# Kernel optimization log

Hardware: AMD Instinct MI355X
Metric: run time of the kernel (lower is better)

Reference implementation:

```python
import jax, jax.numpy as jnp
import numpy as np

B, NVIS, NPIX, W = 16, 65536, 1024, 64
NBLOCKS = NVIS // W
NITER = 10


def setup_inputs() -> dict:
    key = jax.random.key(0)
    ks = jax.random.split(key, 10)
    s = 1.0 / np.sqrt(W)  # torch Linear default init range
    return {
        "y_re": jax.random.normal(ks[0], (B, NVIS), jnp.float32),
        "y_im": jax.random.normal(ks[1], (B, NVIS), jnp.float32),
        "H_re": jax.random.normal(ks[2], (NVIS, NPIX), jnp.float32) / np.sqrt(NPIX),
        "H_im": jax.random.normal(ks[3], (NVIS, NPIX), jnp.float32) / np.sqrt(NPIX),
        "estep_w": jax.random.uniform(ks[4], (W, W), jnp.float32, -s, s),
        "estep_b": jax.random.uniform(ks[5], (W,), jnp.float32, -s, s),
        "update_w": jax.random.uniform(ks[6], (W, W), jnp.float32, -s, s),
        "update_b": jax.random.uniform(ks[7], (W,), jnp.float32, -s, s),
        "memory_w": jax.random.uniform(ks[8], (W, W), jnp.float32, -s, s),
        "memory_b": jax.random.uniform(ks[9], (W,), jnp.float32, -s, s),
        "threshold": jnp.float32(0.001),
        "niter": NITER,
    }


def _forward(y_re, y_im, H_re, H_im, estep_w, estep_b, update_w, update_b,
             memory_w, memory_b, threshold, niter):
    w = estep_w.shape[0]                       # net_width
    batch, nvis = y_re.shape
    nblocks = nvis // w
    y = (y_re + 1j * y_im).reshape(batch, nblocks, w)          # [B, K, W] complex
    H = (H_re + 1j * H_im).reshape(nblocks, w, -1)             # [K, W, P] complex
    npix = H.shape[-1]

    # x0 = sum over blocks of y_k @ H_k  -> [B, P]
    x = jnp.einsum('bkw,kwp->bp', y, H)
    tau = jnp.zeros((batch, nblocks, w), jnp.float32)

    y_k = jnp.swapaxes(y, 0, 1)                                # [K, B, W]

    def block_step(x, inputs):
        Hb, yb, tprev = inputs                                 # [W,P], [B,W], [B,W]
        zk = jnp.einsum('bp,wp->bw', x, Hb.conj())             # [B, W] complex
        r2 = jnp.abs(yb - zk) ** 2                             # [B, W] float
        ht = jax.nn.sigmoid(r2 @ estep_w.T + estep_b)
        wnew = jax.nn.relu(ht @ update_w.T + update_b
                           + tprev @ memory_w.T + memory_b)    # [B, W] float
        zk = zk * wnew.astype(zk.dtype)
        x = x + jnp.einsum('bw,wp->bp', yb - zk, Hb) / w       # residual back-projection
        return x, wnew

    for _ in range(niter):
        tau_k = jnp.swapaxes(tau, 0, 1)                        # [K, B, W]
        x, tau_new = jax.lax.scan(block_step, x, (H, y_k, tau_k))
        tau = jnp.swapaxes(tau_new, 0, 1)
        # global soft-threshold: sgn(x) * relu(|x| - threshold * max|x|)
        absx = jnp.abs(x)
        mag = jax.nn.relu(absx - threshold * jnp.max(absx))
        safe = jnp.where(absx > 0, absx, 1.0)
        sgn = jnp.where(absx > 0, x / safe, 0.0 + 0.0j)
        x = sgn * mag

    return jnp.abs(x)                                          # [B, P] float


def reference(y_re, y_im, H_re, H_im, estep_w, estep_b, update_w, update_b,
              memory_w, memory_b, threshold, niter):
    return _forward(y_re, y_im, H_re, H_im, estep_w, estep_b, update_w,
                    update_b, memory_w, memory_b, threshold, niter)
```

## Files before the change

kernel.cpp:

```cpp
#include <hip/hip_runtime.h>
#include <math.h>

#define NB     16
#define NW     64
#define NK     1024
#define NPX    1024
#define NVIS_  65536
#define NMEM   15
#define TPB    256
#define NWG    256
#define NQP    19

#define WS_ROOTA   0
#define WS_ROOTB   16
#define WS_GMAX    288
#define WS_SRING_W 2048
#define WS_RRING_W 493568
#define WS_X0P_W   526336
#define WS_TAU_W   1574912
#define WS_G_W     2623488
#define INIT_W     526336

#define AG_LDF(p)    __hip_atomic_load((p), __ATOMIC_RELAXED, __HIP_MEMORY_SCOPE_AGENT)
#define AG_STF(p,v)  __hip_atomic_store((p), (v), __ATOMIC_RELAXED, __HIP_MEMORY_SCOPE_AGENT)
#define AG_STU(p,v)  __hip_atomic_store((p), (v), __ATOMIC_RELAXED, __HIP_MEMORY_SCOPE_AGENT)
#define AG_ST64(p,v) __hip_atomic_store((p), (v), __ATOMIC_RELAXED, __HIP_MEMORY_SCOPE_AGENT)

#define BARL() do { asm volatile("s_waitcnt lgkmcnt(0)" ::: "memory"); \
                    __builtin_amdgcn_s_barrier(); } while (0)

typedef struct { float re[NW][NQP][4]; float im[NW][NQP][4]; } HTile;
typedef struct {
  HTile tile[3];
  float xs[160];
  float rs[128];
  float partl[128];
  float red[8][NQP][8];
  float axs[128];
} MemSM;
typedef struct {
  float wE[NW*65], wU[NW*65], wM[NW*65];
  float bE[NW], bU[NW], bM[NW];
  float ztA[128], ztB[128];
  float rloc[2][128];
  float rpost[128];
  float r2s[NW], tpl[NW], hts[NW];
} SeqSM;
typedef struct { float ysr[2048], ysi[2048]; } X0SM;
typedef union { MemSM m; SeqSM q; X0SM x; } SMem;

__global__ void robbi_init(unsigned* ws) {
  for (int i = blockIdx.x * blockDim.x + threadIdx.x; i < INIT_W; i += gridDim.x * blockDim.x)
    __hip_atomic_store(ws + i, 0u, __ATOMIC_RELAXED, __HIP_MEMORY_SCOPE_AGENT);
}

__device__ __forceinline__ void gbar(unsigned* root, unsigned* leaf, int leafmod, unsigned ntarget) {
  __syncthreads();
  if (threadIdx.x == 0) {
    unsigned old = __hip_atomic_fetch_add(leaf, 1u, __ATOMIC_ACQ_REL, __HIP_MEMORY_SCOPE_AGENT);
    if ((old % (unsigned)leafmod) == (unsigned)(leafmod - 1))
      __hip_atomic_fetch_add(root, 1u, __ATOMIC_ACQ_REL, __HIP_MEMORY_SCOPE_AGENT);
    while (__hip_atomic_load(root, __ATOMIC_ACQUIRE, __HIP_MEMORY_SCOPE_AGENT) < ntarget)
      __builtin_amdgcn_s_sleep(4);
  }
  __syncthreads();
}

__global__ __launch_bounds__(256) void robbi_gram(const float* __restrict__ H_re,
                                                  const float* __restrict__ H_im,
                                                  float* ws) {
  const int j = blockIdx.x >> 1;
  const int d = (blockIdx.x & 1) + 1;
  const int k = j + d;
  if (k >= NK) return;
  unsigned* Gu = (unsigned*)ws + WS_G_W;
  const int t = threadIdx.x;
  __shared__ float hj[64 * 130];
  __shared__ float hk[64 * 130];
  const int c = t & 63, wg = t >> 6;
  float accr[16], acci[16];
#pragma unroll
  for (int ii = 0; ii < 16; ++ii) { accr[ii] = 0.f; acci[ii] = 0.f; }
  for (int pc = 0; pc < 16; ++pc) {
    for (int q = t; q < 1024; q += 256) {
      int row = q >> 4, px4 = (q & 15) * 4;
      size_t offj = (size_t)(j * NW + row) * NPX + pc * 64 + px4;
      size_t offk = (size_t)(k * NW + row) * NPX + pc * 64 + px4;
      float4 r4 = *(const float4*)(H_re + offj);
      float4 i4 = *(const float4*)(H_im + offj);
      int b0 = row * 130 + px4 * 2;
      hj[b0+0]=r4.x; hj[b0+1]=i4.x; hj[b0+2]=r4.y; hj[b0+3]=i4.y;
      hj[b0+4]=r4.z; hj[b0+5]=i4.z; hj[b0+6]=r4.w; hj[b0+7]=i4.w;
      r4 = *(const float4*)(H_re + offk);
      i4 = *(const float4*)(H_im + offk);
      hk[b0+0]=r4.x; hk[b0+1]=i4.x; hk[b0+2]=r4.y; hk[b0+3]=i4.y;
      hk[b0+4]=r4.z; hk[b0+5]=i4.z; hk[b0+6]=r4.w; hk[b0+7]=i4.w;
    }
    __syncthreads();
#pragma unroll
    for (int ii = 0; ii < 16; ++ii) {
      const int w = wg * 16 + ii;
      float ar_ = 0.f, ai_ = 0.f;
      for (int px = 0; px < 64; ++px) {
        float jr = hj[w*130 + px*2], ji = hj[w*130 + px*2 + 1];
        float kr = hk[c*130 + px*2], ki = hk[c*130 + px*2 + 1];
        ar_ += jr*kr + ji*ki;
        ai_ += ji*kr - jr*ki;
      }
      accr[ii] += ar_; acci[ii] += ai_;
    }
    __syncthreads();
  }
#pragma unroll
  for (int ii = 0; ii < 16; ++ii) {
    unsigned br = __float_as_uint(accr[ii]);
    br = (br + 0x7FFFu + ((br >> 16) & 1u)) & 0xFFFF0000u;
    unsigned bi = __float_as_uint(acci[ii]);
    bi = ((bi + 0x7FFFu + ((bi >> 16) & 1u)) >> 16) & 0xFFFFu;
    Gu[((size_t)(j * 2 + (d - 1)) * 64 + c) * 64 + wg * 16 + ii] = br | bi;
  }
}

#define GMAC(UU, IDX)                                                           \
  { unsigned uu_ = (UU);                                                        \
    float gr_ = __uint_as_float(uu_ & 0xffff0000u);                             \
    float gi_ = __uint_as_float(uu_ << 16);                                     \
    float rr_ = rl[2*(IDX)], ri_ = rl[2*(IDX)+1];                               \
    ar += rr_*gr_ - ri_*gi_; ai += rr_*gi_ + ri_*gr_; }

__global__ __launch_bounds__(TPB, 1) void robbi_pipe(
    const float* __restrict__ y_re, const float* __restrict__ y_im,
    const float* __restrict__ H_re, const float* __restrict__ H_im,
    const float* __restrict__ Ew, const float* __restrict__ Eb,
    const float* __restrict__ Uw, const float* __restrict__ Ub,
    const float* __restrict__ Mw, const float* __restrict__ Mb,
    const float* __restrict__ thr_p, const int* __restrict__ niter_p,
    float* __restrict__ out, float* ws) {
  const int bid = blockIdx.x;
  const int t = threadIdx.x;
  unsigned* wsu = (unsigned*)ws;
  const unsigned* Gu = wsu + WS_G_W;
  float* tau = ws + WS_TAU_W;
  __shared__ SMem sm;

  const float thr = *thr_p;
  const int niter = *niter_p;
  const int wsub = t >> 5;
  const int g5 = t & 31;
  const int p4 = 4 * g5;

  {
    const int kwc = bid >> 3, ps = bid & 7;
    float ar[2][4], ai[2][4];
#pragma unroll
    for (int h = 0; h < 2; ++h)
#pragma unroll
      for (int j = 0; j < 4; ++j) { ar[h][j] = 0.f; ai[h][j] = 0.f; }
    for (int slab = 0; slab < 16; ++slab) {
      const int kw0 = kwc * 2048 + slab * 128;
      for (int e = t; e < 2048; e += TPB) {
        int bb = e >> 7, j = e & 127;
        sm.x.ysr[e] = y_re[bb * NVIS_ + kw0 + j];
        sm.x.ysi[e] = y_im[bb * NVIS_ + kw0 + j];
      }
      __syncthreads();
      for (int j = 0; j < 128; ++j) {
        const size_t off2 = (size_t)(kw0 + j) * NPX + ps * 128 + p4;
        float4 h4r = *(const float4*)(H_re + off2);
        float4 h4i = *(const float4*)(H_im + off2);
#pragma unroll
        for (int h = 0; h < 2; ++h) {
          int bb = wsub + 8 * h;
          float yr = sm.x.ysr[bb * 128 + j], yi = sm.x.ysi[bb * 128 + j];
          ar[h][0] += yr*h4r.x - yi*h4i.x; ai[h][0] += yr*h4i.x + yi*h4r.x;
          ar[h][1] += yr*h4r.y - yi*h4i.y; ai[h][1] += yr*h4i.y + yi*h4r.y;
          ar[h][2] += yr*h4r.z - yi*h4i.z; ai[h][2] += yr*h4i.z + yi*h4r.z;
          ar[h][3] += yr*h4r.w - yi*h4i.w; ai[h][3] += yr*h4i.w + yi*h4r.w;
        }
      }
      __syncthreads();
    }
#pragma unroll
    for (int h = 0; h < 2; ++h) {
      int bb = wsub + 8 * h;
#pragma unroll
      for (int j = 0; j < 4; ++j) {
        float* pp = ws + WS_X0P_W + ((size_t)((kwc * NB + bb) * NPX + ps * 128 + p4 + j)) * 2;
        AG_STF(pp, ar[h][j]); AG_STF(pp + 1, ai[h][j]);
      }
    }
  }
  gbar(wsu + WS_ROOTA, wsu + 32 * (1 + (bid & 7)), 32, 8u);

  if (bid >= NB * NMEM) {
    const int b = bid - NB * NMEM;
    SeqSM* Q = &sm.q;
    for (int i = t; i < NW * NW; i += TPB) {
      int r = i >> 6, c = i & 63;
      Q->wE[r*65+c] = Ew[i]; Q->wU[r*65+c] = Uw[i]; Q->wM[r*65+c] = Mw[i];
    }
    if (t < NW) { Q->bE[t] = Eb[t]; Q->bU[t] = Ub[t]; Q->bM[t] = Mb[t]; }
    __syncthreads();
    if (niter <= 0) return;

    const int lane = t & 63;
    float ypr = 0.f, ypi = 0.f, tpr = 0.f;
    if (t < 64) { ypr = y_re[b * NVIS_ + t]; ypi = y_im[b * NVIS_ + t]; }
    uint4 g1[16], g2[16];
#pragma unroll
    for (int q2 = 0; q2 < 16; ++q2) { g1[q2] = make_uint4(0,0,0,0); g2[q2] = make_uint4(0,0,0,0); }

    const long NTOT = (long)niter * NK;
    for (long L = 0; L < NTOT; ++L) {
      const int k = (int)(L & (NK - 1));
      const int it2 = (int)(L >> 10);
      float zr = 0.f, zi = 0.f;
      if (t < 64) {
        const unsigned want = (unsigned)L + 1u;
        const int slot8 = (int)(L & 7);
        for (;;) {
          uint4 u[NMEM];
#pragma unroll
          for (int m2 = 0; m2 < NMEM; ++m2) {
            const uint4* p = (const uint4*)(wsu + WS_SRING_W +
              ((size_t)((b * 8 + slot8) * NMEM + m2) * 64 + t) * 4);
            asm volatile("global_load_dwordx4 %0, %1, off sc0 sc1" : "=v"(u[m2]) : "v"(p));
          }
          asm volatile("s_waitcnt vmcnt(0)" ::: "memory");
          __builtin_amdgcn_sched_barrier(0);
          bool ok = true; float ar = 0.f, ai = 0.f;
#pragma unroll
          for (int m2 = 0; m2 < NMEM; ++m2) {
            ok = ok && (u[m2].z == want);
            ar += __uint_as_float(u[m2].x); ai += __uint_as_float(u[m2].y);
          }
          if (__all((int)ok)) { zr = ar; zi = ai; break; }
          __builtin_amdgcn_s_sleep(1);
        }
      } else if (t < 128) {
        if (k >= 1) {
          const float* rl = Q->rloc[(int)((L - 1) & 1)];
          float ar = 0.f, ai = 0.f;
#pragma unroll
          for (int q2 = 0; q2 < 16; ++q2) {
            uint4 u = g1[q2];
            GMAC(u.x, 4*q2+0) GMAC(u.y, 4*q2+1) GMAC(u.z, 4*q2+2) GMAC(u.w, 4*q2+3)
          }
          Q->ztA[2*lane] = ar * (1.f / NW); Q->ztA[2*lane+1] = ai * (1.f / NW);
        }
      } else if (t < 192) {
        if (k >= 2) {
          const float* rl = Q->rloc[(int)((L - 2) & 1)];
          float ar = 0.f, ai = 0.f;
#pragma unroll
          for (int q2 = 0; q2 < 16; ++q2) {
            uint4 u = g2[q2];
            GMAC(u.x, 4*q2+0) GMAC(u.y, 4*q2+1) GMAC(u.z, 4*q2+2) GMAC(u.w, 4*q2+3)
          }
          Q->ztB[2*lane] = ar * (1.f / NW); Q->ztB[2*lane+1] = ai * (1.f / NW);
        }
      } else {
        if (k >= 1) {
          const unsigned Lr = (unsigned)(L - 1);
          union { float2 f2; unsigned long long u; } cv;
          cv.f2 = make_float2(Q->rpost[2*lane], Q->rpost[2*lane+1]);
          unsigned woff = WS_RRING_W + (((b * 8 + (int)(Lr & 7u)) * 64 + lane)) * 4;
          AG_ST64((unsigned long long*)(wsu + woff), cv.u);
          asm volatile("s_waitcnt vmcnt(0)" ::: "memory");
          AG_STU(wsu + woff + 2, Lr + 1u);
        }
      }
      BARL();
      if (t < 64) {
        float z_r = zr, z_i = zi;
        if (k >= 1) { z_r += Q->ztA[2*t]; z_i += Q->ztA[2*t+1]; }
        if (k >= 2) { z_r += Q->ztB[2*t]; z_i += Q->ztB[2*t+1]; }
        float dr = ypr - z_r, di = ypi - z_i;
        Q->r2s[t] = dr*dr + di*di;
        Q->tpl[t] = (it2 == 0) ? 0.f : tpr;
        asm volatile("s_waitcnt lgkmcnt(0)" ::: "memory");
        float e = Q->bE[t];
#pragma unroll 16
        for (int j2 = 0; j2 < 64; ++j2) e += Q->wE[t*65+j2] * Q->r2s[j2];
        Q->hts[t] = 1.f / (1.f + __expf(-e));
        asm volatile("s_waitcnt lgkmcnt(0)" ::: "memory");
        float a = Q->bU[t] + Q->bM[t];
#pragma unroll 16
        for (int j2 = 0; j2 < 64; ++j2)
          a += Q->wU[t*65+j2] * Q->hts[j2] + Q->wM[t*65+j2] * Q->tpl[j2];
        float wn = fmaxf(a, 0.f);
        tau[((size_t)b * NK + k) * NW + t] = wn;
        float rr = ypr - z_r * wn, ri = ypi - z_i * wn;
        Q->rloc[(int)(L & 1)][2*t] = rr; Q->rloc[(int)(L & 1)][2*t+1] = ri;
        Q->rpost[2*t] = rr; Q->rpost[2*t+1] = ri;
        if (L + 1 < NTOT) {
          const int k2 = (int)((L + 1) & (NK - 1));
          ypr = y_re[b * NVIS_ + k2 * NW + t];
          ypi = y_im[b * NVIS_ + k2 * NW + t];
          tpr = tau[((size_t)b * NK + k2) * NW + t];
        }
      } else if (t < 128) {
        if (k + 1 < NK) {
          const unsigned* gp = Gu + ((size_t)(k * 2 + 0) * 64 + lane) * 64;
#pragma unroll
          for (int q2 = 0; q2 < 16; ++q2) g1[q2] = ((const uint4*)gp)[q2];
        }
      } else if (t < 192) {
        if (k + 1 < NK && k >= 1) {
          const unsigned* gp = Gu + ((size_t)((k - 1) * 2 + 1) * 64 + lane) * 64;
#pragma unroll
          for (int q2 = 0; q2 < 16; ++q2) g2[q2] = ((const uint4*)gp)[q2];
        }
      }
      BARL();
      if (k == NK - 1 && t >= 192) {
        union { float2 f2; unsigned long long u; } cv;
        cv.f2 = make_float2(Q->rpost[2*lane], Q->rpost[2*lane+1]);
        unsigned woff = WS_RRING_W + (((b * 8 + (int)(L & 7u)) * 64 + lane)) * 4;
        AG_ST64((unsigned long long*)(wsu + woff), cv.u);
        asm volatile("s_waitcnt vmcnt(0)" ::: "memory");
        AG_STU(wsu + woff + 2, (unsigned)L + 1u);
      }
    }
    return;
  }

  const int b = bid / NMEM;
  const int m = bid % NMEM;
  const int off = m * 68;
  const int cnt = (m == NMEM - 1) ? 72 : 68;
  const int nq = cnt >> 2;
  MemSM* M = &sm.m;

  if (t < cnt * 2) {
    int p = t >> 1, c = t & 1;
    float s = 0.f;
    for (int kwc = 0; kwc < 32; ++kwc)
      s += AG_LDF(ws + WS_X0P_W + ((size_t)((kwc * NB + b) * NPX + off + p)) * 2 + c);
    M->xs[2 * p + c] = s;
  }
  __syncthreads();

  if (niter <= 0) {
    if (t < cnt) {
      float xr = M->xs[2*t], xi = M->xs[2*t+1];
      out[b * NPX + off + t] = sqrtf(xr*xr + xi*xi);
    }
    return;
  }

  float4 hr[8], hi[8];

  auto load_tile = [&](int k) {
    if (g5 < nq) {
      const size_t rb = ((size_t)k * NW + wsub) * NPX + off + p4;
#pragma unroll
      for (int i = 0; i < 8; ++i) {
        hr[i] = *(const float4*)(H_re + rb + (size_t)i * 8 * NPX);
        hi[i] = *(const float4*)(H_im + rb + (size_t)i * 8 * NPX);
      }
    }
  };
  auto store_tile = [&](int slot) {
    if (g5 < nq) {
#pragma unroll
      for (int i = 0; i < 8; ++i) {
        int w = 8 * i + wsub;
        *(float4*)&M->tile[slot].re[w][g5][0] = hr[i];
        *(float4*)&M->tile[slot].im[w][g5][0] = hi[i];
      }
    }
  };
  auto compute_A = [&]() {
    float zpr[8], zpi[8];
    float4 xq0 = make_float4(0,0,0,0), xq1 = make_float4(0,0,0,0);
    if (g5 < nq) { xq0 = *(const float4*)&M->xs[p4*2]; xq1 = *(const float4*)&M->xs[p4*2+4]; }
#pragma unroll
    for (int i = 0; i < 8; ++i) {
      float zr = 0.f, zi = 0.f;
      if (g5 < nq) {
        zr = xq0.x*hr[i].x + xq0.y*hi[i].x + xq0.z*hr[i].y + xq0.w*hi[i].y
           + xq1.x*hr[i].z + xq1.y*hi[i].z + xq1.z*hr[i].w + xq1.w*hi[i].w;
        zi = xq0.y*hr[i].x - xq0.x*hi[i].x + xq0.w*hr[i].y - xq0.z*hi[i].y
           + xq1.y*hr[i].z - xq1.x*hi[i].z + xq1.w*hr[i].w - xq1.z*hi[i].w;
      }
#pragma unroll
      for (int msk = 16; msk >= 1; msk >>= 1) {
        zr += __shfl_xor(zr, msk); zi += __shfl_xor(zi, msk);
      }
      zpr[i] = zr; zpi[i] = zi;
    }
    if (g5 == 0) {
#pragma unroll
      for (int i = 0; i < 8; ++i) {
        M->partl[(8*i + wsub)*2]     = zpr[i];
        M->partl[(8*i + wsub)*2 + 1] = zpi[i];
      }
    }
  };
  auto post_s = [&](unsigned Ls) {
    const int slot8 = (int)(Ls & 7u);
    union { float2 f2; unsigned long long u; } cv;
    cv.f2 = make_float2(M->partl[2*t], M->partl[2*t+1]);
    unsigned woff = WS_SRING_W + ((size_t)((b * 8 + slot8) * NMEM + m) * 64 + t) * 4;
    AG_ST64((unsigned long long*)(wsu + woff), cv.u);
    asm volatile("s_waitcnt vmcnt(0)" ::: "memory");
    AG_STU(wsu + woff + 2, Ls + 1u);
  };
  auto poll_r = [&](unsigned Lr) {
    const int l = t - 64;
    const unsigned want = Lr + 1u;
    const uint4* p = (const uint4*)(wsu + WS_RRING_W +
        ((size_t)((b * 8 + (int)(Lr & 7u)) * 64 + l)) * 4);
    uint4 u;
    for (;;) {
      asm volatile("global_load_dwordx4 %0, %1, off sc0 sc1\n\ts_waitcnt vmcnt(0)"
                   : "=v"(u) : "v"(p) : "memory");
      if (__all((int)(u.z == want))) break;
      __builtin_amdgcn_s_sleep(1);
    }
    M->rs[2*l]   = __uint_as_float(u.x);
    M->rs[2*l+1] = __uint_as_float(u.y);
  };

  for (int iter = 0; iter < niter; ++iter) {
    const unsigned L0 = (unsigned)(iter * NK);
    for (int kk = 0; kk < 3; ++kk) {
      load_tile(kk);
      compute_A();
      BARL();
      if (t < 64) post_s(L0 + kk);
      store_tile(kk);
      BARL();
    }
    load_tile(3);
    if (t >= 64 && t < 128) poll_r(L0);
    BARL();

    for (int j = 0; j < NK; ++j) {
      const int slot = j % 3;
      if (g5 < nq) {
        float dre[4] = {0,0,0,0}, dim[4] = {0,0,0,0};
#pragma unroll
        for (int i = 0; i < 8; ++i) {
          int w = 8*i + wsub;
          float rr = M->rs[2*w], ri = M->rs[2*w+1];
          float4 re4 = *(const float4*)&M->tile[slot].re[w][g5][0];
          float4 im4 = *(const float4*)&M->tile[slot].im[w][g5][0];
          dre[0] += rr*re4.x - ri*im4.x; dim[0] += rr*im4.x + ri*re4.x;
          dre[1] += rr*re4.y - ri*im4.y; dim[1] += rr*im4.y + ri*re4.y;
          dre[2] += rr*re4.z - ri*im4.z; dim[2] += rr*im4.z + ri*re4.z;
          dre[3] += rr*re4.w - ri*im4.w; dim[3] += rr*im4.w + ri*re4.w;
        }
#pragma unroll
        for (int e = 0; e < 4; ++e) {
          M->red[wsub][g5][2*e]   = dre[e];
          M->red[wsub][g5][2*e+1] = dim[e];
        }
      }
      BARL();
      if (t < cnt * 2) {
        int p = t >> 1, c = t & 1;
        float s = 0.f;
#pragma unroll
        for (int u2 = 0; u2 < 8; ++u2) s += M->red[u2][p >> 2][(p & 3) * 2 + c];
        M->xs[2*p + c] += s * (1.f / NW);
      }
      BARL();
      const int ka = j + 3;
      if (ka < NK) compute_A();
      BARL();
      if (ka < NK) {
        if (t < 64) post_s(L0 + (unsigned)ka);
        store_tile(slot);
      }
      if (ka + 1 < NK) load_tile(ka + 1);
      if (j + 1 < NK) { if (t >= 64 && t < 128) poll_r(L0 + (unsigned)(j + 1)); }
      BARL();
    }

    {
      float ax = 0.f;
      if (t < cnt) {
        float xr = M->xs[2*t], xi = M->xs[2*t+1];
        ax = sqrtf(xr*xr + xi*xi);
        M->axs[t] = ax;
      } else if (t < 128) M->axs[t] = 0.f;
      __syncthreads();
      for (int o = 64; o > 0; o >>= 1) {
        if (t < o) M->axs[t] = fmaxf(M->axs[t], M->axs[t + o]);
        __syncthreads();
      }
      if (t == 0)
        __hip_atomic_fetch_max(wsu + WS_GMAX + (iter & 63), __float_as_uint(M->axs[0]),
                               __ATOMIC_RELAXED, __HIP_MEMORY_SCOPE_AGENT);
      gbar(wsu + WS_ROOTB, wsu + 512 + 32 * (bid & 7), 30, 8u * (unsigned)(iter + 1));
      float gm = __uint_as_float(__hip_atomic_load(wsu + WS_GMAX + (iter & 63),
                                 __ATOMIC_RELAXED, __HIP_MEMORY_SCOPE_AGENT));
      if (t < cnt) {
        float mag = fmaxf(ax - thr * gm, 0.f);
        float sc = (ax > 0.f) ? (mag / ax) : 0.f;
        M->xs[2*t] *= sc; M->xs[2*t+1] *= sc;
        if (iter == niter - 1) out[b * NPX + off + t] = mag;
      }
      __syncthreads();
    }
  }
}

extern "C" void kernel_launch(void* const* d_in, const int* in_sizes, int n_in,
                              void* d_out, int out_size, void* d_ws, size_t ws_size,
                              hipStream_t stream) {
  const float* y_re = (const float*)d_in[0];
  const float* y_im = (const float*)d_in[1];
  const float* H_re = (const float*)d_in[2];
  const float* H_im = (const float*)d_in[3];
  const float* Ew   = (const float*)d_in[4];
  const float* Eb   = (const float*)d_in[5];
  const float* Uw   = (const float*)d_in[6];
  const float* Ub   = (const float*)d_in[7];
  const float* Mw   = (const float*)d_in[8];
  const float* Mb   = (const float*)d_in[9];
  const float* thr  = (const float*)d_in[10];
  const int*  niter = (const int*)d_in[11];
  (void)in_sizes; (void)n_in; (void)out_size; (void)ws_size;

  robbi_init<<<512, 256, 0, stream>>>((unsigned*)d_ws);
  robbi_gram<<<NK * 2, 256, 0, stream>>>(H_re, H_im, (float*)d_ws);
  robbi_pipe<<<NWG, TPB, 0, stream>>>(
      y_re, y_im, H_re, H_im, Ew, Eb, Uw, Ub, Mw, Mb, thr, niter,
      (float*)d_out, (float*)d_ws);
}
```

Before: 55.81 ms.

## Widen Gram-correction window to 4 blocks and stream H tiles via registers

The Gram kernel now computes four off-diagonal block couplings (d=1..4) per block instead of two, so the sequential per-batch workgroup can correct z for the four most recent residuals across three waves. This widens the pipelining window between memory workgroups and the sequential chain from 3 to 5 blocks. Memory workgroups drop the LDS H tile ring and instead hold the H tiles in registers for both the forward projection and the back-projection, double-buffering the residual. Sequential-ring loads are prefetched a step ahead. The cost is more Gram precompute, more register pressure, and more redundant global H reads.

```diff
diff --git a/kernel.cpp b/kernel.cpp
--- a/kernel.cpp
+++ b/kernel.cpp
@@ -9,11 +9,13 @@
 #define NMEM   15
 #define TPB    256
 #define NWG    256
-#define NQP    19
+#define WWIN   5
+#define NDC    4
 
 #define WS_ROOTA   0
 #define WS_ROOTB   16
 #define WS_GMAX    288
+#define WS_LEAFB   512
 #define WS_SRING_W 2048
 #define WS_RRING_W 493568
 #define WS_X0P_W   526336
@@ -29,20 +31,20 @@
 #define BARL() do { asm volatile("s_waitcnt lgkmcnt(0)" ::: "memory"); \
                     __builtin_amdgcn_s_barrier(); } while (0)
 
-typedef struct { float re[NW][NQP][4]; float im[NW][NQP][4]; } HTile;
+#define ESTR 164
+
 typedef struct {
-  HTile tile[3];
   float xs[160];
-  float rs[128];
+  float rsbuf[2][128];
   float partl[128];
-  float red[8][NQP][8];
+  float redc[8 * ESTR];
   float axs[128];
 } MemSM;
 typedef struct {
-  float wE[NW*65], wU[NW*65], wM[NW*65];
+  float wE[NW * 65], wU[NW * 65], wM[NW * 65];
   float bE[NW], bU[NW], bM[NW];
   float ztA[128], ztB[128];
-  float rloc[2][128];
+  float rloc[4][128];
   float rpost[128];
   float r2s[NW], tpl[NW], hts[NW];
 } SeqSM;
@@ -70,62 +72,82 @@
                                                   const float* __restrict__ H_im,
                                                   float* ws) {
   const int j = blockIdx.x >> 1;
-  const int d = (blockIdx.x & 1) + 1;
-  const int k = j + d;
-  if (k >= NK) return;
+  const int d0 = 1 + 2 * (blockIdx.x & 1);
   unsigned* Gu = (unsigned*)ws + WS_G_W;
   const int t = threadIdx.x;
   __shared__ float hj[64 * 130];
   __shared__ float hk[64 * 130];
   const int c = t & 63, wg = t >> 6;
-  float accr[16], acci[16];
-#pragma unroll
-  for (int ii = 0; ii < 16; ++ii) { accr[ii] = 0.f; acci[ii] = 0.f; }
+  float accr[2][16], acci[2][16];
+#pragma unroll
+  for (int dd = 0; dd < 2; ++dd)
+#pragma unroll
+    for (int ii = 0; ii < 16; ++ii) { accr[dd][ii] = 0.f; acci[dd][ii] = 0.f; }
+
   for (int pc = 0; pc < 16; ++pc) {
     for (int q = t; q < 1024; q += 256) {
       int row = q >> 4, px4 = (q & 15) * 4;
       size_t offj = (size_t)(j * NW + row) * NPX + pc * 64 + px4;
-      size_t offk = (size_t)(k * NW + row) * NPX + pc * 64 + px4;
       float4 r4 = *(const float4*)(H_re + offj);
       float4 i4 = *(const float4*)(H_im + offj);
       int b0 = row * 130 + px4 * 2;
       hj[b0+0]=r4.x; hj[b0+1]=i4.x; hj[b0+2]=r4.y; hj[b0+3]=i4.y;
       hj[b0+4]=r4.z; hj[b0+5]=i4.z; hj[b0+6]=r4.w; hj[b0+7]=i4.w;
-      r4 = *(const float4*)(H_re + offk);
-      i4 = *(const float4*)(H_im + offk);
-      hk[b0+0]=r4.x; hk[b0+1]=i4.x; hk[b0+2]=r4.y; hk[b0+3]=i4.y;
-      hk[b0+4]=r4.z; hk[b0+5]=i4.z; hk[b0+6]=r4.w; hk[b0+7]=i4.w;
-    }
-    __syncthreads();
-#pragma unroll
-    for (int ii = 0; ii < 16; ++ii) {
-      const int w = wg * 16 + ii;
-      float ar_ = 0.f, ai_ = 0.f;
-      for (int px = 0; px < 64; ++px) {
-        float jr = hj[w*130 + px*2], ji = hj[w*130 + px*2 + 1];
-        float kr = hk[c*130 + px*2], ki = hk[c*130 + px*2 + 1];
-        ar_ += jr*kr + ji*ki;
-        ai_ += ji*kr - jr*ki;
-      }
-      accr[ii] += ar_; acci[ii] += ai_;
-    }
-    __syncthreads();
-  }
-#pragma unroll
-  for (int ii = 0; ii < 16; ++ii) {
-    unsigned br = __float_as_uint(accr[ii]);
-    br = (br + 0x7FFFu + ((br >> 16) & 1u)) & 0xFFFF0000u;
-    unsigned bi = __float_as_uint(acci[ii]);
-    bi = ((bi + 0x7FFFu + ((bi >> 16) & 1u)) >> 16) & 0xFFFFu;
-    Gu[((size_t)(j * 2 + (d - 1)) * 64 + c) * 64 + wg * 16 + ii] = br | bi;
+    }
+#pragma unroll
+    for (int dd = 0; dd < 2; ++dd) {
+      const int k = j + d0 + dd;
+      if (k < NK) {
+        for (int q = t; q < 1024; q += 256) {
+          int row = q >> 4, px4 = (q & 15) * 4;
+          size_t offk = (size_t)(k * NW + row) * NPX + pc * 64 + px4;
+          float4 r4 = *(const float4*)(H_re + offk);
+          float4 i4 = *(const float4*)(H_im + offk);
+          int b0 = row * 130 + px4 * 2;
+          hk[b0+0]=r4.x; hk[b0+1]=i4.x; hk[b0+2]=r4.y; hk[b0+3]=i4.y;
+          hk[b0+4]=r4.z; hk[b0+5]=i4.z; hk[b0+6]=r4.w; hk[b0+7]=i4.w;
+        }
+      }
+      __syncthreads();
+      if (k < NK) {
+#pragma unroll
+        for (int ii = 0; ii < 16; ++ii) {
+          const int w = wg * 16 + ii;
+          float ar_ = 0.f, ai_ = 0.f;
+#pragma unroll 8
+          for (int px = 0; px < 64; ++px) {
+            float jr = hj[w*130 + px*2], ji = hj[w*130 + px*2 + 1];
+            float kr = hk[c*130 + px*2], ki = hk[c*130 + px*2 + 1];
+            ar_ += jr*kr + ji*ki;
+            ai_ += ji*kr - jr*ki;
+          }
+          accr[dd][ii] += ar_; acci[dd][ii] += ai_;
+        }
+      }
+      __syncthreads();
+    }
+  }
+#pragma unroll
+  for (int dd = 0; dd < 2; ++dd) {
+    const int k = j + d0 + dd;
+    if (k < NK) {
+#pragma unroll
+      for (int ii = 0; ii < 16; ++ii) {
+        unsigned br = __float_as_uint(accr[dd][ii]);
+        br = (br + 0x7FFFu + ((br >> 16) & 1u)) & 0xFFFF0000u;
+        unsigned bi = __float_as_uint(acci[dd][ii]);
+        bi = ((bi + 0x7FFFu + ((bi >> 16) & 1u)) >> 16) & 0xFFFFu;
+        Gu[((size_t)(j * NDC + (d0 + dd - 1)) * 64 + c) * 64 + wg * 16 + ii] = br | bi;
+      }
+    }
   }
 }
 
-#define GMAC(UU, IDX)                                                           \
+#define GMAC(UU, IDX, RL)                                                       \
   { unsigned uu_ = (UU);                                                        \
     float gr_ = __uint_as_float(uu_ & 0xffff0000u);                             \
     float gi_ = __uint_as_float(uu_ << 16);                                     \
-    float rr_ = rl[2*(IDX)], ri_ = rl[2*(IDX)+1];                               \
+    float rr_ = (RL)[2*(IDX)], ri_ = (RL)[2*(IDX)+1];                           \
     ar += rr_*gr_ - ri_*gi_; ai += rr_*gi_ + ri_*gr_; }
 
 __global__ __launch_bounds__(TPB, 1) void robbi_pipe(
@@ -203,64 +225,96 @@
     __syncthreads();
     if (niter <= 0) return;
 
-    const int lane = t & 63;
+    const int wv = t >> 6, lane = t & 63;
     float ypr = 0.f, ypi = 0.f, tpr = 0.f;
-    if (t < 64) { ypr = y_re[b * NVIS_ + t]; ypi = y_im[b * NVIS_ + t]; }
-    uint4 g1[16], g2[16];
-#pragma unroll
-    for (int q2 = 0; q2 < 16; ++q2) { g1[q2] = make_uint4(0,0,0,0); g2[q2] = make_uint4(0,0,0,0); }
+    uint4 su[NMEM];
+    uint4 gA[16], gB[16];
+#pragma unroll
+    for (int q2 = 0; q2 < 16; ++q2) { gA[q2] = make_uint4(0,0,0,0); gB[q2] = make_uint4(0,0,0,0); }
+#pragma unroll
+    for (int m2 = 0; m2 < NMEM; ++m2) su[m2] = make_uint4(0,0,0,0);
+
+    if (wv == 0) {
+      ypr = y_re[b * NVIS_ + lane];
+      ypi = y_im[b * NVIS_ + lane];
+#pragma unroll
+      for (int m2 = 0; m2 < NMEM; ++m2) {
+        const uint4* p = (const uint4*)(wsu + WS_SRING_W +
+            ((size_t)((b * 8 + 0) * NMEM + m2) * 64 + lane) * 4);
+        asm volatile("global_load_dwordx4 %0, %1, off sc0 sc1" : "=v"(su[m2]) : "v"(p));
+      }
+    }
 
     const long NTOT = (long)niter * NK;
     for (long L = 0; L < NTOT; ++L) {
       const int k = (int)(L & (NK - 1));
       const int it2 = (int)(L >> 10);
       float zr = 0.f, zi = 0.f;
-      if (t < 64) {
+      if (wv == 0) {
         const unsigned want = (unsigned)L + 1u;
         const int slot8 = (int)(L & 7);
+        bool first = true;
         for (;;) {
-          uint4 u[NMEM];
-#pragma unroll
-          for (int m2 = 0; m2 < NMEM; ++m2) {
-            const uint4* p = (const uint4*)(wsu + WS_SRING_W +
-              ((size_t)((b * 8 + slot8) * NMEM + m2) * 64 + t) * 4);
-            asm volatile("global_load_dwordx4 %0, %1, off sc0 sc1" : "=v"(u[m2]) : "v"(p));
+          if (!first) {
+#pragma unroll
+            for (int m2 = 0; m2 < NMEM; ++m2) {
+              const uint4* p = (const uint4*)(wsu + WS_SRING_W +
+                  ((size_t)((b * 8 + slot8) * NMEM + m2) * 64 + lane) * 4);
+              asm volatile("global_load_dwordx4 %0, %1, off sc0 sc1" : "=v"(su[m2]) : "v"(p));
+            }
           }
           asm volatile("s_waitcnt vmcnt(0)" ::: "memory");
           __builtin_amdgcn_sched_barrier(0);
           bool ok = true; float ar = 0.f, ai = 0.f;
 #pragma unroll
           for (int m2 = 0; m2 < NMEM; ++m2) {
-            ok = ok && (u[m2].z == want);
-            ar += __uint_as_float(u[m2].x); ai += __uint_as_float(u[m2].y);
+            ok = ok && (su[m2].z == want);
+            ar += __uint_as_float(su[m2].x); ai += __uint_as_float(su[m2].y);
           }
           if (__all((int)ok)) { zr = ar; zi = ai; break; }
+          first = false;
           __builtin_amdgcn_s_sleep(1);
         }
-      } else if (t < 128) {
+      } else if (wv == 1) {
+        float ar = 0.f, ai = 0.f;
         if (k >= 1) {
-          const float* rl = Q->rloc[(int)((L - 1) & 1)];
-          float ar = 0.f, ai = 0.f;
+          const float* rl = Q->rloc[(int)((L - 1) & 3)];
 #pragma unroll
           for (int q2 = 0; q2 < 16; ++q2) {
-            uint4 u = g1[q2];
-            GMAC(u.x, 4*q2+0) GMAC(u.y, 4*q2+1) GMAC(u.z, 4*q2+2) GMAC(u.w, 4*q2+3)
-          }
-          Q->ztA[2*lane] = ar * (1.f / NW); Q->ztA[2*lane+1] = ai * (1.f / NW);
-        }
-      } else if (t < 192) {
+            uint4 u = gA[q2];
+            GMAC(u.x, 4*q2+0, rl) GMAC(u.y, 4*q2+1, rl) GMAC(u.z, 4*q2+2, rl) GMAC(u.w, 4*q2+3, rl)
+          }
+        }
         if (k >= 2) {
-          const float* rl = Q->rloc[(int)((L - 2) & 1)];
-          float ar = 0.f, ai = 0.f;
+          const float* rl = Q->rloc[(int)((L - 2) & 3)];
 #pragma unroll
           for (int q2 = 0; q2 < 16; ++q2) {
-            uint4 u = g2[q2];
-            GMAC(u.x, 4*q2+0) GMAC(u.y, 4*q2+1) GMAC(u.z, 4*q2+2) GMAC(u.w, 4*q2+3)
-          }
-          Q->ztB[2*lane] = ar * (1.f / NW); Q->ztB[2*lane+1] = ai * (1.f / NW);
-        }
+            uint4 u = gB[q2];
+            GMAC(u.x, 4*q2+0, rl) GMAC(u.y, 4*q2+1, rl) GMAC(u.z, 4*q2+2, rl) GMAC(u.w, 4*q2+3, rl)
+          }
+        }
+        Q->ztA[2*lane] = ar * (1.f / NW); Q->ztA[2*lane+1] = ai * (1.f / NW);
+      } else if (wv == 2) {
+        float ar = 0.f, ai = 0.f;
+        if (k >= 3) {
+          const float* rl = Q->rloc[(int)((L - 3) & 3)];
+#pragma unroll
+          for (int q2 = 0; q2 < 16; ++q2) {
+            uint4 u = gA[q2];
+            GMAC(u.x, 4*q2+0, rl) GMAC(u.y, 4*q2+1, rl) GMAC(u.z, 4*q2+2, rl) GMAC(u.w, 4*q2+3, rl)
+          }
+        }
+        if (k >= 4) {
+          const float* rl = Q->rloc[(int)((L - 4) & 3)];
+#pragma unroll
+          for (int q2 = 0; q2 < 16; ++q2) {
+            uint4 u = gB[q2];
+            GMAC(u.x, 4*q2+0, rl) GMAC(u.y, 4*q2+1, rl) GMAC(u.z, 4*q2+2, rl) GMAC(u.w, 4*q2+3, rl)
+          }
+        }
+        Q->ztB[2*lane] = ar * (1.f / NW); Q->ztB[2*lane+1] = ai * (1.f / NW);
       } else {
-        if (k >= 1) {
+        if (L >= 1) {
           const unsigned Lr = (unsigned)(L - 1);
           union { float2 f2; unsigned long long u; } cv;
           cv.f2 = make_float2(Q->rpost[2*lane], Q->rpost[2*lane+1]);
@@ -271,10 +325,9 @@
         }
       }
       BARL();
-      if (t < 64) {
-        float z_r = zr, z_i = zi;
-        if (k >= 1) { z_r += Q->ztA[2*t]; z_i += Q->ztA[2*t+1]; }
-        if (k >= 2) { z_r += Q->ztB[2*t]; z_i += Q->ztB[2*t+1]; }
+      if (wv == 0) {
+        float z_r = zr + Q->ztA[2*t] + Q->ztB[2*t];
+        float z_i = zi + Q->ztA[2*t+1] + Q->ztB[2*t+1];
         float dr = ypr - z_r, di = ypi - z_i;
         Q->r2s[t] = dr*dr + di*di;
         Q->tpl[t] = (it2 == 0) ? 0.f : tpr;
@@ -291,29 +344,48 @@
         float wn = fmaxf(a, 0.f);
         tau[((size_t)b * NK + k) * NW + t] = wn;
         float rr = ypr - z_r * wn, ri = ypi - z_i * wn;
-        Q->rloc[(int)(L & 1)][2*t] = rr; Q->rloc[(int)(L & 1)][2*t+1] = ri;
+        Q->rloc[(int)(L & 3)][2*t] = rr; Q->rloc[(int)(L & 3)][2*t+1] = ri;
         Q->rpost[2*t] = rr; Q->rpost[2*t+1] = ri;
         if (L + 1 < NTOT) {
           const int k2 = (int)((L + 1) & (NK - 1));
           ypr = y_re[b * NVIS_ + k2 * NW + t];
           ypi = y_im[b * NVIS_ + k2 * NW + t];
           tpr = tau[((size_t)b * NK + k2) * NW + t];
-        }
-      } else if (t < 128) {
-        if (k + 1 < NK) {
-          const unsigned* gp = Gu + ((size_t)(k * 2 + 0) * 64 + lane) * 64;
-#pragma unroll
-          for (int q2 = 0; q2 < 16; ++q2) g1[q2] = ((const uint4*)gp)[q2];
-        }
-      } else if (t < 192) {
-        if (k + 1 < NK && k >= 1) {
-          const unsigned* gp = Gu + ((size_t)((k - 1) * 2 + 1) * 64 + lane) * 64;
-#pragma unroll
-          for (int q2 = 0; q2 < 16; ++q2) g2[q2] = ((const uint4*)gp)[q2];
-        }
-      }
-      BARL();
-      if (k == NK - 1 && t >= 192) {
+          const int slotn = (int)((L + 1) & 7);
+#pragma unroll
+          for (int m2 = 0; m2 < NMEM; ++m2) {
+            const uint4* p = (const uint4*)(wsu + WS_SRING_W +
+                ((size_t)((b * 8 + slotn) * NMEM + m2) * 64 + lane) * 4);
+            asm volatile("global_load_dwordx4 %0, %1, off sc0 sc1" : "=v"(su[m2]) : "v"(p));
+          }
+        }
+      } else if (wv == 1) {
+        const int kn = (int)((L + 1) & (NK - 1));
+        if (L + 1 < NTOT && kn >= 1) {
+          const uint4* gp = (const uint4*)(Gu + ((size_t)((kn - 1) * NDC + 0) * 64 + lane) * 64);
+#pragma unroll
+          for (int q2 = 0; q2 < 16; ++q2) gA[q2] = gp[q2];
+        }
+        if (L + 1 < NTOT && kn >= 2) {
+          const uint4* gp = (const uint4*)(Gu + ((size_t)((kn - 2) * NDC + 1) * 64 + lane) * 64);
+#pragma unroll
+          for (int q2 = 0; q2 < 16; ++q2) gB[q2] = gp[q2];
+        }
+      } else if (wv == 2) {
+        const int kn = (int)((L + 1) & (NK - 1));
+        if (L + 1 < NTOT && kn >= 3) {
+          const uint4* gp = (const uint4*)(Gu + ((size_t)((kn - 3) * NDC + 2) * 64 + lane) * 64);
+#pragma unroll
+          for (int q2 = 0; q2 < 16; ++q2) gA[q2] = gp[q2];
+        }
+        if (L + 1 < NTOT && kn >= 4) {
+          const uint4* gp = (const uint4*)(Gu + ((size_t)((kn - 4) * NDC + 3) * 64 + lane) * 64);
+#pragma unroll
+          for (int q2 = 0; q2 < 16; ++q2) gB[q2] = gp[q2];
+        }
+      }
+      BARL();
+      if (k == NK - 1 && wv == 3) {
         union { float2 f2; unsigned long long u; } cv;
         cv.f2 = make_float2(Q->rpost[2*lane], Q->rpost[2*lane+1]);
         unsigned woff = WS_RRING_W + (((b * 8 + (int)(L & 7u)) * 64 + lane)) * 4;
@@ -349,25 +421,26 @@
     return;
   }
 
-  float4 hr[8], hi[8];
-
-  auto load_tile = [&](int k) {
+  float4 cr[8], ci[8];
+  float4 ar8[8], ai8[8];
+
+  auto load_C = [&](int k) {
     if (g5 < nq) {
       const size_t rb = ((size_t)k * NW + wsub) * NPX + off + p4;
 #pragma unroll
       for (int i = 0; i < 8; ++i) {
-        hr[i] = *(const float4*)(H_re + rb + (size_t)i * 8 * NPX);
-        hi[i] = *(const float4*)(H_im + rb + (size_t)i * 8 * NPX);
+        cr[i] = *(const float4*)(H_re + rb + (size_t)i * 8 * NPX);
+        ci[i] = *(const float4*)(H_im + rb + (size_t)i * 8 * NPX);
       }
     }
   };
-  auto store_tile = [&](int slot) {
+  auto load_A = [&](int k) {
     if (g5 < nq) {
+      const size_t rb = ((size_t)k * NW + wsub) * NPX + off + p4;
 #pragma unroll
       for (int i = 0; i < 8; ++i) {
-        int w = 8 * i + wsub;
-        *(float4*)&M->tile[slot].re[w][g5][0] = hr[i];
-        *(float4*)&M->tile[slot].im[w][g5][0] = hi[i];
+        ar8[i] = *(const float4*)(H_re + rb + (size_t)i * 8 * NPX);
+        ai8[i] = *(const float4*)(H_im + rb + (size_t)i * 8 * NPX);
       }
     }
   };
@@ -379,10 +452,10 @@
     for (int i = 0; i < 8; ++i) {
       float zr = 0.f, zi = 0.f;
       if (g5 < nq) {
-        zr = xq0.x*hr[i].x + xq0.y*hi[i].x + xq0.z*hr[i].y + xq0.w*hi[i].y
-           + xq1.x*hr[i].z + xq1.y*hi[i].z + xq1.z*hr[i].w + xq1.w*hi[i].w;
-        zi = xq0.y*hr[i].x - xq0.x*hi[i].x + xq0.w*hr[i].y - xq0.z*hi[i].y
-           + xq1.y*hr[i].z - xq1.x*hi[i].z + xq1.w*hr[i].w - xq1.z*hi[i].w;
+        zr = xq0.x*ar8[i].x + xq0.y*ai8[i].x + xq0.z*ar8[i].y + xq0.w*ai8[i].y
+           + xq1.x*ar8[i].z + xq1.y*ai8[i].z + xq1.z*ar8[i].w + xq1.w*ai8[i].w;
+        zi = xq0.y*ar8[i].x - xq0.x*ai8[i].x + xq0.w*ar8[i].y - xq0.z*ai8[i].y
+           + xq1.y*ar8[i].z - xq1.x*ai8[i].z + xq1.w*ar8[i].w - xq1.z*ai8[i].w;
       }
 #pragma unroll
       for (int msk = 16; msk >= 1; msk >>= 1) {
@@ -407,7 +480,7 @@
     asm volatile("s_waitcnt vmcnt(0)" ::: "memory");
     AG_STU(wsu + woff + 2, Ls + 1u);
   };
-  auto poll_r = [&](unsigned Lr) {
+  auto poll_r = [&](unsigned Lr, int buf) {
     const int l = t - 64;
     const unsigned want = Lr + 1u;
     const uint4* p = (const uint4*)(wsu + WS_RRING_W +
@@ -419,43 +492,42 @@
       if (__all((int)(u.z == want))) break;
       __builtin_amdgcn_s_sleep(1);
     }
-    M->rs[2*l]   = __uint_as_float(u.x);
-    M->rs[2*l+1] = __uint_as_float(u.y);
+    M->rsbuf[buf][2*l]   = __uint_as_float(u.x);
+    M->rsbuf[buf][2*l+1] = __uint_as_float(u.y);
   };
 
   for (int iter = 0; iter < niter; ++iter) {
     const unsigned L0 = (unsigned)(iter * NK);
-    for (int kk = 0; kk < 3; ++kk) {
-      load_tile(kk);
+    for (int kk = 0; kk < WWIN; ++kk) {
+      load_A(kk);
       compute_A();
       BARL();
-      if (t < 64) post_s(L0 + kk);
-      store_tile(kk);
-      BARL();
-    }
-    load_tile(3);
-    if (t >= 64 && t < 128) poll_r(L0);
+      if (t < 64) post_s(L0 + (unsigned)kk);
+      BARL();
+    }
+    load_C(0);
+    load_A(WWIN);
+    if (t >= 64 && t < 128) poll_r(L0, 0);
     BARL();
 
     for (int j = 0; j < NK; ++j) {
-      const int slot = j % 3;
+      const int cur = j & 1;
       if (g5 < nq) {
+        const float* rsb = M->rsbuf[cur];
         float dre[4] = {0,0,0,0}, dim[4] = {0,0,0,0};
 #pragma unroll
         for (int i = 0; i < 8; ++i) {
           int w = 8*i + wsub;
-          float rr = M->rs[2*w], ri = M->rs[2*w+1];
-          float4 re4 = *(const float4*)&M->tile[slot].re[w][g5][0];
-          float4 im4 = *(const float4*)&M->tile[slot].im[w][g5][0];
-          dre[0] += rr*re4.x - ri*im4.x; dim[0] += rr*im4.x + ri*re4.x;
-          dre[1] += rr*re4.y - ri*im4.y; dim[1] += rr*im4.y + ri*re4.y;
-          dre[2] += rr*re4.z - ri*im4.z; dim[2] += rr*im4.z + ri*re4.z;
-          dre[3] += rr*re4.w - ri*im4.w; dim[3] += rr*im4.w + ri*re4.w;
-        }
-#pragma unroll
-        for (int e = 0; e < 4; ++e) {
-          M->red[wsub][g5][2*e]   = dre[e];
-          M->red[wsub][g5][2*e+1] = dim[e];
+          float rr = rsb[2*w], ri = rsb[2*w+1];
+          dre[0] += rr*cr[i].x - ri*ci[i].x; dim[0] += rr*ci[i].x + ri*cr[i].x;
+          dre[1] += rr*cr[i].y - ri*ci[i].y; dim[1] += rr*ci[i].y + ri*cr[i].y;
+          dre[2] += rr*cr[i].z - ri*ci[i].z; dim[2] += rr*ci[i].z + ri*cr[i].z;
+          dre[3] += rr*cr[i].w - ri*ci[i].w; dim[3] += rr*ci[i].w + ri*cr[i].w;
+        }
+#pragma unroll
+        for (int q = 0; q < 4; ++q) {
+          M->redc[(2*q)   * ESTR + wsub*20 + g5] = dre[q];
+          M->redc[(2*q+1) * ESTR + wsub*20 + g5] = dim[q];
         }
       }
       BARL();
@@ -463,19 +535,18 @@
         int p = t >> 1, c = t & 1;
         float s = 0.f;
 #pragma unroll
-        for (int u2 = 0; u2 < 8; ++u2) s += M->red[u2][p >> 2][(p & 3) * 2 + c];
+        for (int u2 = 0; u2 < 8; ++u2)
+          s += M->redc[((p & 3)*2 + c) * ESTR + u2*20 + (p >> 2)];
         M->xs[2*p + c] += s * (1.f / NW);
       }
       BARL();
-      const int ka = j + 3;
+      const int ka = j + WWIN;
       if (ka < NK) compute_A();
       BARL();
-      if (ka < NK) {
-        if (t < 64) post_s(L0 + (unsigned)ka);
-        store_tile(slot);
-      }
-      if (ka + 1 < NK) load_tile(ka + 1);
-      if (j + 1 < NK) { if (t >= 64 && t < 128) poll_r(L0 + (unsigned)(j + 1)); }
+      if (ka < NK && t < 64) post_s(L0 + (unsigned)ka);
+      if (j + 1 < NK && t >= 64 && t < 128) poll_r(L0 + (unsigned)(j + 1), (j + 1) & 1);
+      if (j + 1 < NK) load_C(j + 1);
+      if (ka + 1 < NK) load_A(ka + 1);
       BARL();
     }
 
@@ -494,7 +565,7 @@
       if (t == 0)
         __hip_atomic_fetch_max(wsu + WS_GMAX + (iter & 63), __float_as_uint(M->axs[0]),
                                __ATOMIC_RELAXED, __HIP_MEMORY_SCOPE_AGENT);
-      gbar(wsu + WS_ROOTB, wsu + 512 + 32 * (bid & 7), 30, 8u * (unsigned)(iter + 1));
+      gbar(wsu + WS_ROOTB, wsu + WS_LEAFB + 32 * (bid & 7), 30, 8u * (unsigned)(iter + 1));
       float gm = __uint_as_float(__hip_atomic_load(wsu + WS_GMAX + (iter & 63),
                                  __ATOMIC_RELAXED, __HIP_MEMORY_SCOPE_AGENT));
       if (t < cnt) {
```

Measured after the change: 66.90 ms. 19.9% more time.
